# Performance work log

Measured on AMD Instinct MI355X. Metric: run time of the kernel, lower is better.

## Reference

```python
import jax, jax.numpy as jnp
import numpy as np

EPS = 1e-6

def rmsnorm(x, w):
    return x * jax.lax.rsqrt(jnp.mean(x * x, axis=-1, keepdims=True) + EPS) * w

def hard_sigmoid(x):
    # relu6(x + 3) / 6 - 0.5
    return jnp.clip(x + 3.0, 0.0, 6.0) / 6.0 - 0.5

def setup_inputs() -> dict:
    key = jax.random.key(0)
    ks = jax.random.split(key, 8)
    B, T, C, E = 4, 4096, 1024, 4
    H = E * C
    x = jax.random.normal(ks[0], (B, T, C), dtype=jnp.float32)
    norm1_w = jnp.ones((C,), dtype=jnp.float32)
    norm2_w = jnp.ones((C,), dtype=jnp.float32)
    s1 = 1.0 / np.sqrt(C)
    s2 = 1.0 / np.sqrt(H)
    mlp1_w = jax.random.uniform(ks[1], (C, C), jnp.float32, -s1, s1)
    mlp1_b = jax.random.uniform(ks[2], (C,), jnp.float32, -s1, s1)
    mlp2a_w = jax.random.uniform(ks[3], (C, H), jnp.float32, -s1, s1)
    mlp2a_b = jax.random.uniform(ks[4], (H,), jnp.float32, -s1, s1)
    mlp2b_w = jax.random.uniform(ks[5], (H, C), jnp.float32, -s2, s2)
    mlp2b_b = jax.random.uniform(ks[6], (C,), jnp.float32, -s2, s2)
    return {"x": x, "norm1_w": norm1_w, "mlp1_w": mlp1_w, "mlp1_b": mlp1_b,
            "norm2_w": norm2_w, "mlp2a_w": mlp2a_w, "mlp2a_b": mlp2a_b,
            "mlp2b_w": mlp2b_w, "mlp2b_b": mlp2b_b}

def reference(x, norm1_w, mlp1_w, mlp1_b, norm2_w, mlp2a_w, mlp2a_b, mlp2b_w, mlp2b_b):
    # state: [B, T, C] prefix sum over time of gated, normalized input
    state = jnp.cumsum(hard_sigmoid(rmsnorm(x, norm1_w)), axis=1)
    out = hard_sigmoid(state @ mlp1_w + mlp1_b) * x
    h = jax.nn.relu(rmsnorm(out, norm2_w) @ mlp2a_w + mlp2a_b)
    return h @ mlp2b_w + mlp2b_b + out
```

## Files before the change

### kernel.cpp

```cpp
#include <hip/hip_runtime.h>

#define B_     4
#define T_     4096
#define C_     1024
#define H_     4096
#define BT_    (B_ * T_)
#define NCH_   64
#define CHLEN_ 64
#define MCHUNK 8192

typedef __bf16 bf16_t;
typedef __bf16 bf16x8 __attribute__((ext_vector_type(8)));
typedef float  f32x4  __attribute__((ext_vector_type(4)));

__device__ __forceinline__ float hs_f(float v) {
    return fminf(fmaxf((v + 3.0f) * (1.0f / 6.0f), 0.0f), 1.0f) - 0.5f;
}

__device__ __forceinline__ void gld_lds16(const bf16_t* g, bf16_t* l) {
    __builtin_amdgcn_global_load_lds((const __attribute__((address_space(1))) void*)g,
                                     (__attribute__((address_space(3))) void*)l,
                                     16, 0, 0);
}

__global__ __launch_bounds__(256) void rms_rows_f32(const float* __restrict__ X,
                                                    float* __restrict__ inv) {
    const int wave = threadIdx.x >> 6, lane = threadIdx.x & 63;
    const int row = blockIdx.x * 4 + wave;
    const float* xr = X + (size_t)row * C_;
    float s = 0.0f;
    #pragma unroll
    for (int p = 0; p < 4; p++) {
        float4 v = *(const float4*)(xr + p * 256 + lane * 4);
        s += v.x * v.x + v.y * v.y + v.z * v.z + v.w * v.w;
    }
    #pragma unroll
    for (int o = 32; o > 0; o >>= 1) s += __shfl_down(s, o, 64);
    if (lane == 0) inv[row] = rsqrtf(s * (1.0f / C_) + 1e-6f);
}

__global__ __launch_bounds__(256) void rms_rows_bf16(const bf16_t* __restrict__ X,
                                                     float* __restrict__ inv) {
    const int wave = threadIdx.x >> 6, lane = threadIdx.x & 63;
    const int row = blockIdx.x * 4 + wave;
    const bf16_t* xr = X + (size_t)row * C_;
    bf16x8 v0 = *(const bf16x8*)(xr + lane * 8);
    bf16x8 v1 = *(const bf16x8*)(xr + 512 + lane * 8);
    float s = 0.0f;
    #pragma unroll
    for (int j = 0; j < 8; j++) {
        float a = (float)v0[j], b = (float)v1[j];
        s += a * a + b * b;
    }
    #pragma unroll
    for (int o = 32; o > 0; o >>= 1) s += __shfl_down(s, o, 64);
    if (lane == 0) inv[row] = rsqrtf(s * (1.0f / C_) + 1e-6f);
}

__global__ __launch_bounds__(256) void scan_emit_local(const float* __restrict__ X,
                                                       const float* __restrict__ inv1,
                                                       const float* __restrict__ nw,
                                                       bf16_t* __restrict__ state,
                                                       float* __restrict__ csum) {
    const int bch = blockIdx.x;
    const int b = bch >> 6, ch = bch & 63;
    const int c = blockIdx.y * 256 + threadIdx.x;
    const float wgt = nw[c];
    const int rbase = b * T_ + ch * CHLEN_;
    const size_t xbase = (size_t)rbase * C_ + c;
    float acc = 0.0f;
    for (int i = 0; i < CHLEN_; i++) {
        acc += hs_f(X[xbase + (size_t)i * C_] * inv1[rbase + i] * wgt);
        state[(size_t)(rbase + i) * C_ + c] = (bf16_t)acc;
    }
    csum[(size_t)bch * C_ + c] = acc;
}

__global__ __launch_bounds__(256) void scan_offsets_hilo(const float* __restrict__ csum,
                                                         bf16_t* __restrict__ hilo) {
    const int idx = blockIdx.x * 256 + threadIdx.x;
    const int b = idx >> 10, c = idx & 1023;
    const size_t base = (size_t)b * NCH_ * C_ + c;
    float v[NCH_];
    #pragma unroll
    for (int ch = 0; ch < NCH_; ch++)
        v[ch] = csum[base + (size_t)ch * C_];
    float run = 0.0f;
    #pragma unroll
    for (int ch = 0; ch < NCH_; ch++) {
        const size_t row = (size_t)(b * NCH_ + ch) * 2048 + c;
        const bf16_t hi = (bf16_t)run;
        hilo[row] = hi;
        hilo[row + 1024] = (bf16_t)(run - (float)hi);
        run += v[ch];
    }
}

__global__ __launch_bounds__(256) void pmat_init(const float* __restrict__ b1,
                                                 float* __restrict__ Pmat) {
    const int i = blockIdx.x * 256 + threadIdx.x;
    Pmat[i] = b1[i & (C_ - 1)];
}

__global__ __launch_bounds__(256) void transpose_scale(const float* __restrict__ src,
                                                       bf16_t* __restrict__ dst,
                                                       int K, int N, int ldd, int dupOff,
                                                       const float* __restrict__ scale) {
    __shared__ float tile[32][33];
    const int n0 = blockIdx.x * 32, k0 = blockIdx.y * 32;
    const int tx = threadIdx.x & 31, ty = threadIdx.x >> 5;
    #pragma unroll
    for (int j = 0; j < 4; j++) {
        const int kk = ty + j * 8;
        float v = src[(size_t)(k0 + kk) * N + n0 + tx];
        if (scale) v *= scale[k0 + kk];
        tile[kk][tx] = v;
    }
    __syncthreads();
    #pragma unroll
    for (int j = 0; j < 4; j++) {
        const int nn = ty + j * 8;
        const bf16_t v = (bf16_t)tile[tx][nn];
        dst[(size_t)(n0 + nn) * ldd + k0 + tx] = v;
        if (dupOff) dst[(size_t)(n0 + nn) * ldd + dupOff + k0 + tx] = v;
    }
}

template <int MODE, typename ET, typename OT>
__global__ __launch_bounds__(256) void gemm_bt(const bf16_t* __restrict__ A,
                                               const bf16_t* __restrict__ Bt,
                                               const float* __restrict__ bias,
                                               const ET* __restrict__ extra,
                                               const float* __restrict__ rowscale,
                                               const float* __restrict__ pmat,
                                               OT* __restrict__ Cmat,
                                               int N, int K, int lda, int ldb) {
    __shared__ __align__(16) bf16_t As[2][128 * 32];
    __shared__ __align__(16) bf16_t Bs[2][128 * 32];
    const int tid = threadIdx.x;

    const int nwgx = gridDim.x;
    const int flat0 = blockIdx.y * nwgx + blockIdx.x;
    int mTile, nTile;
    if ((nwgx & 7) == 0) {
        const int xcd = flat0 & 7;
        const int loc = flat0 >> 3;
        const int mpx = nwgx >> 3;
        mTile = xcd * mpx + (loc % mpx);
        nTile = loc / mpx;
    } else {
        mTile = blockIdx.x;
        nTile = blockIdx.y;
    }
    const int mBase = mTile * 128;
    const int nBase = nTile * 128;
    const size_t kOff = (size_t)blockIdx.z * K;

    const int wave = tid >> 6;
    const int lane = tid & 63;
    const int waveM = (wave & 1) * 64;
    const int waveN = (wave >> 1) * 64;
    const int lr = lane & 15;
    const int lq = lane >> 4;

    f32x4 acc[4][4] = {};

    const int e0 = tid * 8;
    const int r0 = e0 >> 5, c0 = (((e0 >> 3) & 3) ^ ((r0 >> 1) & 3)) << 3;
    const int e1 = 2048 + tid * 8;
    const int r1 = e1 >> 5, c1 = (((e1 >> 3) & 3) ^ ((r1 >> 1) & 3)) << 3;

    const bf16_t* Ag0 = A + (size_t)(mBase + r0) * lda + kOff + c0;
    const bf16_t* Ag1 = A + (size_t)(mBase + r1) * lda + kOff + c1;
    const bf16_t* Bg0 = Bt + (size_t)(nBase + r0) * ldb + kOff + c0;
    const bf16_t* Bg1 = Bt + (size_t)(nBase + r1) * ldb + kOff + c1;

    auto stage = [&](int buf, int kb) {
        gld_lds16(Ag0 + kb, As[buf] + e0);
        gld_lds16(Ag1 + kb, As[buf] + e1);
        gld_lds16(Bg0 + kb, Bs[buf] + e0);
        gld_lds16(Bg1 + kb, Bs[buf] + e1);
    };

    stage(0, 0);
    if (32 < K) stage(1, 32);

    int cur = 0;
    for (int kb = 0; kb < K; kb += 32) {
        if (kb + 32 < K) asm volatile("s_waitcnt vmcnt(4)" ::: "memory");
        else             asm volatile("s_waitcnt vmcnt(0)" ::: "memory");
        __builtin_amdgcn_s_barrier();

        bf16x8 af[4], bfr[4];
        #pragma unroll
        for (int mi = 0; mi < 4; mi++) {
            const int R = waveM + mi * 16 + lr;
            af[mi] = *(const bf16x8*)(As[cur] + R * 32 + ((lq ^ ((R >> 1) & 3)) << 3));
        }
        #pragma unroll
        for (int ni = 0; ni < 4; ni++) {
            const int R = waveN + ni * 16 + lr;
            bfr[ni] = *(const bf16x8*)(Bs[cur] + R * 32 + ((lq ^ ((R >> 1) & 3)) << 3));
        }
        #pragma unroll
        for (int mi = 0; mi < 4; mi++)
            #pragma unroll
            for (int ni = 0; ni < 4; ni++)
                acc[mi][ni] = __builtin_amdgcn_mfma_f32_16x16x32_bf16(
                    af[mi], bfr[ni], acc[mi][ni], 0, 0, 0);

        __builtin_amdgcn_s_barrier();
        if (kb + 64 < K) stage(cur, kb + 64);
        cur ^= 1;
    }

    #pragma unroll
    for (int ni = 0; ni < 4; ni++) {
        const int n = nBase + waveN + ni * 16 + lr;
        const float bz = (MODE == 1 || MODE == 2) ? bias[n] : 0.0f;
        #pragma unroll
        for (int mi = 0; mi < 4; mi++) {
            #pragma unroll
            for (int r = 0; r < 4; r++) {
                const int m = mBase + waveM + mi * 16 + lq * 4 + r;
                float v = acc[mi][ni][r];
                if (MODE == 0) {
                    v = hs_f(v + pmat[(size_t)(m >> 6) * N + n]) * (float)extra[(size_t)m * N + n];
                    Cmat[(size_t)m * N + n] = (OT)v;
                } else if (MODE == 1) {
                    v = fmaxf(rowscale[m] * v + bz, 0.0f);
                    Cmat[(size_t)m * N + n] = (OT)v;
                } else if (MODE == 2) {
                    v = v + bz + (float)extra[(size_t)m * N + n];
                    Cmat[(size_t)m * N + n] = (OT)v;
                } else {
                    atomicAdd((float*)&Cmat[(size_t)m * N + n], v);
                }
            }
        }
    }
}

extern "C" void kernel_launch(void* const* d_in, const int* in_sizes, int n_in,
                              void* d_out, int out_size, void* d_ws, size_t ws_size,
                              hipStream_t stream) {
    const float* x   = (const float*)d_in[0];
    const float* n1w = (const float*)d_in[1];
    const float* w1  = (const float*)d_in[2];
    const float* b1  = (const float*)d_in[3];
    const float* n2w = (const float*)d_in[4];
    const float* w2a = (const float*)d_in[5];
    const float* b2a = (const float*)d_in[6];
    const float* w2b = (const float*)d_in[7];
    const float* b2b = (const float*)d_in[8];
    float* y = (float*)d_out;

    char* w = (char*)d_ws;
    float*  inv1  = (float*)(w + 0);
    float*  inv2  = (float*)(w + 65536);
    float*  csum  = (float*)(w + 131072);
    bf16_t* hilo  = (bf16_t*)(w + 1179648);
    float*  Pmat  = (float*)(w + 2228224);
    bf16_t* W1cat = (bf16_t*)(w + 5373952);
    bf16_t* W2at  = (bf16_t*)(w + 9568256);
    bf16_t* W2bt  = (bf16_t*)(w + 17956864);
    bf16_t* outb  = (bf16_t*)(w + 26345472);
    bf16_t* state = (bf16_t*)(w + 59899904);
    bf16_t* hbuf  = state;

    rms_rows_f32<<<dim3(BT_ / 4), dim3(256), 0, stream>>>(x, inv1);
    scan_emit_local<<<dim3(B_ * NCH_, C_ / 256), dim3(256), 0, stream>>>(x, inv1, n1w, state, csum);
    scan_offsets_hilo<<<dim3(B_ * C_ / 256), dim3(256), 0, stream>>>(csum, hilo);
    transpose_scale<<<dim3(C_ / 32, C_ / 32), dim3(256), 0, stream>>>(
        w1, W1cat, C_, C_, 2048, 1024, nullptr);
    transpose_scale<<<dim3(H_ / 32, C_ / 32), dim3(256), 0, stream>>>(
        w2a, W2at, C_, H_, C_, 0, n2w);
    transpose_scale<<<dim3(C_ / 32, H_ / 32), dim3(256), 0, stream>>>(
        w2b, W2bt, H_, C_, H_, 0, nullptr);
    pmat_init<<<dim3(256 * C_ / 256), dim3(256), 0, stream>>>(b1, Pmat);
    gemm_bt<4, float, float><<<dim3(2, C_ / 128, 4), dim3(256), 0, stream>>>(
        hilo, W1cat, nullptr, nullptr, nullptr, nullptr, Pmat, C_, 512, 2048, 2048);
    gemm_bt<0, float, bf16_t><<<dim3(BT_ / 128, C_ / 128), dim3(256), 0, stream>>>(
        state, W1cat, nullptr, x, nullptr, Pmat, outb, C_, C_, C_, 2048);
    rms_rows_bf16<<<dim3(BT_ / 4), dim3(256), 0, stream>>>(outb, inv2);
    for (int c = 0; c < BT_ / MCHUNK; c++) {
        const bf16_t* Ao = outb + (size_t)c * MCHUNK * C_;
        float* yo = y + (size_t)c * MCHUNK * C_;
        gemm_bt<1, float, bf16_t><<<dim3(MCHUNK / 128, H_ / 128), dim3(256), 0, stream>>>(
            Ao, W2at, b2a, nullptr, inv2 + c * MCHUNK, nullptr, hbuf, H_, C_, C_, C_);
        gemm_bt<2, bf16_t, float><<<dim3(MCHUNK / 128, C_ / 128), dim3(256), 0, stream>>>(
            hbuf, W2bt, b2b, Ao, nullptr, nullptr, yo, C_, H_, H_, H_);
    }
}
```

Measured before the change: 607.2 us.

## Fuse second RMS sum-of-squares into GEMM epilogue and merge transpose launches

The MODE 0 GEMM epilogue now accumulates per-row sums of squares of the rounded bf16 outputs, reduces them across lanes and atomically adds them to a buffer. A tiny kernel then turns those sums into inverse RMS values, which replaces the separate pass that re-read the whole bf16 activation. The three weight transposes are merged into one launch, and launch bounds gain a min-waves hint (4 or 5) per GEMM mode. The risks are extra atomics and register pressure in the epilogue, and possible spills from the tighter occupancy hints.

```diff
diff --git a/kernel.cpp b/kernel.cpp
--- a/kernel.cpp
+++ b/kernel.cpp
@@ -33,24 +33,6 @@
     for (int p = 0; p < 4; p++) {
         float4 v = *(const float4*)(xr + p * 256 + lane * 4);
         s += v.x * v.x + v.y * v.y + v.z * v.z + v.w * v.w;
-    }
-    #pragma unroll
-    for (int o = 32; o > 0; o >>= 1) s += __shfl_down(s, o, 64);
-    if (lane == 0) inv[row] = rsqrtf(s * (1.0f / C_) + 1e-6f);
-}
-
-__global__ __launch_bounds__(256) void rms_rows_bf16(const bf16_t* __restrict__ X,
-                                                     float* __restrict__ inv) {
-    const int wave = threadIdx.x >> 6, lane = threadIdx.x & 63;
-    const int row = blockIdx.x * 4 + wave;
-    const bf16_t* xr = X + (size_t)row * C_;
-    bf16x8 v0 = *(const bf16x8*)(xr + lane * 8);
-    bf16x8 v1 = *(const bf16x8*)(xr + 512 + lane * 8);
-    float s = 0.0f;
-    #pragma unroll
-    for (int j = 0; j < 8; j++) {
-        float a = (float)v0[j], b = (float)v1[j];
-        s += a * a + b * b;
     }
     #pragma unroll
     for (int o = 32; o > 0; o >>= 1) s += __shfl_down(s, o, 64);
@@ -97,17 +79,46 @@
 }
 
 __global__ __launch_bounds__(256) void pmat_init(const float* __restrict__ b1,
-                                                 float* __restrict__ Pmat) {
+                                                 float* __restrict__ Pmat,
+                                                 float* __restrict__ rs2) {
     const int i = blockIdx.x * 256 + threadIdx.x;
     Pmat[i] = b1[i & (C_ - 1)];
-}
-
-__global__ __launch_bounds__(256) void transpose_scale(const float* __restrict__ src,
-                                                       bf16_t* __restrict__ dst,
-                                                       int K, int N, int ldd, int dupOff,
-                                                       const float* __restrict__ scale) {
+    if (i < BT_) rs2[i] = 0.0f;
+}
+
+__global__ __launch_bounds__(256) void inv_finish(const float* __restrict__ rs2,
+                                                  float* __restrict__ inv) {
+    const int i = blockIdx.x * 256 + threadIdx.x;
+    inv[i] = rsqrtf(rs2[i] * (1.0f / C_) + 1e-6f);
+}
+
+__global__ __launch_bounds__(256) void transpose_all(const float* __restrict__ w1,
+                                                     const float* __restrict__ w2a,
+                                                     const float* __restrict__ w2b,
+                                                     const float* __restrict__ n2w,
+                                                     bf16_t* __restrict__ W1cat,
+                                                     bf16_t* __restrict__ W2at,
+                                                     bf16_t* __restrict__ W2bt) {
     __shared__ float tile[32][33];
-    const int n0 = blockIdx.x * 32, k0 = blockIdx.y * 32;
+    const int flat = blockIdx.x;
+    const float* src; bf16_t* dst; const float* scale;
+    int N, ldd, dupOff, bx, by;
+    if (flat < 1024) {
+        src = w1; dst = W1cat; scale = nullptr;
+        N = C_; ldd = 2048; dupOff = 1024;
+        bx = flat & 31; by = flat >> 5;
+    } else if (flat < 5120) {
+        const int f = flat - 1024;
+        src = w2a; dst = W2at; scale = n2w;
+        N = H_; ldd = C_; dupOff = 0;
+        bx = f & 127; by = f >> 7;
+    } else {
+        const int f = flat - 5120;
+        src = w2b; dst = W2bt; scale = nullptr;
+        N = C_; ldd = H_; dupOff = 0;
+        bx = f & 31; by = f >> 5;
+    }
+    const int n0 = bx * 32, k0 = by * 32;
     const int tx = threadIdx.x & 31, ty = threadIdx.x >> 5;
     #pragma unroll
     for (int j = 0; j < 4; j++) {
@@ -126,15 +137,16 @@
     }
 }
 
-template <int MODE, typename ET, typename OT>
-__global__ __launch_bounds__(256) void gemm_bt(const bf16_t* __restrict__ A,
-                                               const bf16_t* __restrict__ Bt,
-                                               const float* __restrict__ bias,
-                                               const ET* __restrict__ extra,
-                                               const float* __restrict__ rowscale,
-                                               const float* __restrict__ pmat,
-                                               OT* __restrict__ Cmat,
-                                               int N, int K, int lda, int ldb) {
+template <int MODE, int MINW, typename ET, typename OT>
+__global__ __launch_bounds__(256, MINW) void gemm_bt(const bf16_t* __restrict__ A,
+                                                     const bf16_t* __restrict__ Bt,
+                                                     const float* __restrict__ bias,
+                                                     const ET* __restrict__ extra,
+                                                     const float* __restrict__ rowscale,
+                                                     const float* __restrict__ pmat,
+                                                     float* __restrict__ aux,
+                                                     OT* __restrict__ Cmat,
+                                                     int N, int K, int lda, int ldb) {
     __shared__ __align__(16) bf16_t As[2][128 * 32];
     __shared__ __align__(16) bf16_t Bs[2][128 * 32];
     const int tid = threadIdx.x;
@@ -214,6 +226,13 @@
         cur ^= 1;
     }
 
+    float sq[4][4];
+    if (MODE == 0) {
+        #pragma unroll
+        for (int a = 0; a < 4; a++)
+            #pragma unroll
+            for (int b = 0; b < 4; b++) sq[a][b] = 0.0f;
+    }
     #pragma unroll
     for (int ni = 0; ni < 4; ni++) {
         const int n = nBase + waveN + ni * 16 + lr;
@@ -226,7 +245,10 @@
                 float v = acc[mi][ni][r];
                 if (MODE == 0) {
                     v = hs_f(v + pmat[(size_t)(m >> 6) * N + n]) * (float)extra[(size_t)m * N + n];
-                    Cmat[(size_t)m * N + n] = (OT)v;
+                    const OT vs = (OT)v;
+                    Cmat[(size_t)m * N + n] = vs;
+                    const float vb = (float)vs;
+                    sq[mi][r] += vb * vb;
                 } else if (MODE == 1) {
                     v = fmaxf(rowscale[m] * v + bz, 0.0f);
                     Cmat[(size_t)m * N + n] = (OT)v;
@@ -235,6 +257,23 @@
                     Cmat[(size_t)m * N + n] = (OT)v;
                 } else {
                     atomicAdd((float*)&Cmat[(size_t)m * N + n], v);
+                }
+            }
+        }
+    }
+    if (MODE == 0) {
+        #pragma unroll
+        for (int mi = 0; mi < 4; mi++) {
+            #pragma unroll
+            for (int r = 0; r < 4; r++) {
+                float s = sq[mi][r];
+                s += __shfl_xor(s, 1, 64);
+                s += __shfl_xor(s, 2, 64);
+                s += __shfl_xor(s, 4, 64);
+                s += __shfl_xor(s, 8, 64);
+                if (lr == 0) {
+                    const int m = mBase + waveM + mi * 16 + lq * 4 + r;
+                    atomicAdd(&aux[m], s);
                 }
             }
         }
@@ -267,28 +306,25 @@
     bf16_t* outb  = (bf16_t*)(w + 26345472);
     bf16_t* state = (bf16_t*)(w + 59899904);
     bf16_t* hbuf  = state;
+    float*  rs2   = csum;
 
     rms_rows_f32<<<dim3(BT_ / 4), dim3(256), 0, stream>>>(x, inv1);
     scan_emit_local<<<dim3(B_ * NCH_, C_ / 256), dim3(256), 0, stream>>>(x, inv1, n1w, state, csum);
     scan_offsets_hilo<<<dim3(B_ * C_ / 256), dim3(256), 0, stream>>>(csum, hilo);
-    transpose_scale<<<dim3(C_ / 32, C_ / 32), dim3(256), 0, stream>>>(
-        w1, W1cat, C_, C_, 2048, 1024, nullptr);
-    transpose_scale<<<dim3(H_ / 32, C_ / 32), dim3(256), 0, stream>>>(
-        w2a, W2at, C_, H_, C_, 0, n2w);
-    transpose_scale<<<dim3(C_ / 32, H_ / 32), dim3(256), 0, stream>>>(
-        w2b, W2bt, H_, C_, H_, 0, nullptr);
-    pmat_init<<<dim3(256 * C_ / 256), dim3(256), 0, stream>>>(b1, Pmat);
-    gemm_bt<4, float, float><<<dim3(2, C_ / 128, 4), dim3(256), 0, stream>>>(
-        hilo, W1cat, nullptr, nullptr, nullptr, nullptr, Pmat, C_, 512, 2048, 2048);
-    gemm_bt<0, float, bf16_t><<<dim3(BT_ / 128, C_ / 128), dim3(256), 0, stream>>>(
-        state, W1cat, nullptr, x, nullptr, Pmat, outb, C_, C_, C_, 2048);
-    rms_rows_bf16<<<dim3(BT_ / 4), dim3(256), 0, stream>>>(outb, inv2);
+    transpose_all<<<dim3(9216), dim3(256), 0, stream>>>(
+        w1, w2a, w2b, n2w, W1cat, W2at, W2bt);
+    pmat_init<<<dim3(256 * C_ / 256), dim3(256), 0, stream>>>(b1, Pmat, rs2);
+    gemm_bt<4, 4, float, float><<<dim3(2, C_ / 128, 4), dim3(256), 0, stream>>>(
+        hilo, W1cat, nullptr, nullptr, nullptr, nullptr, nullptr, Pmat, C_, 512, 2048, 2048);
+    gemm_bt<0, 4, float, bf16_t><<<dim3(BT_ / 128, C_ / 128), dim3(256), 0, stream>>>(
+        state, W1cat, nullptr, x, nullptr, Pmat, rs2, outb, C_, C_, C_, 2048);
+    inv_finish<<<dim3(BT_ / 256), dim3(256), 0, stream>>>(rs2, inv2);
     for (int c = 0; c < BT_ / MCHUNK; c++) {
         const bf16_t* Ao = outb + (size_t)c * MCHUNK * C_;
         float* yo = y + (size_t)c * MCHUNK * C_;
-        gemm_bt<1, float, bf16_t><<<dim3(MCHUNK / 128, H_ / 128), dim3(256), 0, stream>>>(
-            Ao, W2at, b2a, nullptr, inv2 + c * MCHUNK, nullptr, hbuf, H_, C_, C_, C_);
-        gemm_bt<2, bf16_t, float><<<dim3(MCHUNK / 128, C_ / 128), dim3(256), 0, stream>>>(
-            hbuf, W2bt, b2b, Ao, nullptr, nullptr, yo, C_, H_, H_, H_);
-    }
-}
+        gemm_bt<1, 5, float, bf16_t><<<dim3(MCHUNK / 128, H_ / 128), dim3(256), 0, stream>>>(
+            Ao, W2at, b2a, nullptr, inv2 + c * MCHUNK, nullptr, nullptr, hbuf, H_, C_, C_, C_);
+        gemm_bt<2, 5, bf16_t, float><<<dim3(MCHUNK / 128, C_ / 128), dim3(256), 0, stream>>>(
+            hbuf, W2bt, b2b, Ao, nullptr, nullptr, nullptr, yo, C_, H_, H_, H_);
+    }
+}
```

Result: slower. 1.141 ms (+87.9%).
